# Performance work log

Measured on AMD Instinct MI355X. Metric: run time of the kernel, lower is better.

The kernel has to match this reference:

```python
import jax, jax.numpy as jnp
import numpy as np

H = 2048       # hidden_size
F = 1024       # moe_intermediate_size
E = 32         # n_routed_experts
G = 8          # n_group
TOPK_GROUP = 3
TOP_K = 6      # num_experts_per_tok
N_SHARED = 2
SCALE = 1.0    # routed_scaling_factor
B, S = 1, 2048


def setup_inputs() -> dict:
    key = jax.random.key(0)
    ks = jax.random.split(key, 8)
    std = 0.02
    return {
        "hidden_states": jax.random.normal(ks[0], (B, S, H), dtype=jnp.float32),
        "w_gate": jax.random.normal(ks[1], (E, H), dtype=jnp.float32) * std,
        "wg": jax.random.normal(ks[2], (E, H, F), dtype=jnp.float32) * std,  # stacked gate_proj
        "wu": jax.random.normal(ks[3], (E, H, F), dtype=jnp.float32) * std,  # stacked up_proj
        "wd": jax.random.normal(ks[4], (E, F, H), dtype=jnp.float32) * std,  # stacked down_proj
        "sg": jax.random.normal(ks[5], (N_SHARED * F, H), dtype=jnp.float32) * std,  # shared gate_proj
        "su": jax.random.normal(ks[6], (N_SHARED * F, H), dtype=jnp.float32) * std,  # shared up_proj
        "sd": jax.random.normal(ks[7], (H, N_SHARED * F), dtype=jnp.float32) * std,  # shared down_proj
    }


def reference(hidden_states, w_gate, wg, wu, wd, sg, su, sd):
    b, s, h = hidden_states.shape
    x = hidden_states.reshape(-1, h)                    # [T, H]
    T = x.shape[0]

    # ---- MoEGate (softmax scoring, group_limited_greedy top-k) ----
    logits = x.astype(jnp.float32) @ w_gate.T           # [T, E]
    scores = jax.nn.softmax(logits, axis=-1)
    group_scores = scores.reshape(T, G, E // G).max(axis=-1)          # [T, G]
    _, group_idx = jax.lax.top_k(group_scores, TOPK_GROUP)            # [T, topk_group]
    group_mask = jax.nn.one_hot(group_idx, G, dtype=scores.dtype).sum(axis=1)  # [T, G]
    score_mask = jnp.repeat(group_mask, E // G, axis=-1)              # [T, E]
    tmp_scores = jnp.where(score_mask > 0.5, scores, 0.0)
    topk_weight, topk_idx = jax.lax.top_k(tmp_scores, TOP_K)          # [T, K]
    # norm_topk_prob=True, top_k>1
    topk_weight = topk_weight / (topk_weight.sum(axis=-1, keepdims=True) + 1e-20) * SCALE

    # combine weights per (token, expert): scatter topk weights (indices distinct)
    combine_w = jnp.zeros((T, E), dtype=jnp.float32)
    combine_w = combine_w.at[jnp.arange(T)[:, None], topk_idx].add(topk_weight)

    # ---- routed experts: dense grouped GEMMs, weighted combine ----
    g = jnp.einsum('th,ehf->etf', x, wg)                # [E, T, F]
    u = jnp.einsum('th,ehf->etf', x, wu)                # [E, T, F]
    act = jax.nn.silu(g) * u                            # SiLU gated
    act = act * combine_w.T[:, :, None]                 # fold combine weights before down-proj
    y = jnp.einsum('etf,efh->th', act, wd)              # [T, H]

    # ---- shared experts ----
    shared = (jax.nn.silu(x @ sg.T) * (x @ su.T)) @ sd.T

    return (y + shared).reshape(b, s, h)
```

## Files before the change

kernel.cpp:

```cpp
#include <hip/hip_runtime.h>

#define HD   2048
#define FD   1024
#define NEXP 32
#define TOPK 6
#define TT   2048
#define SDIM 2048
#define NPAIR (TT*TOPK)
#define BSTR 40

typedef __bf16 bf16x8 __attribute__((ext_vector_type(8)));
typedef float  f32x4  __attribute__((ext_vector_type(4)));

#define GLOAD_LDS16(g, l) __builtin_amdgcn_global_load_lds( \
    (const __attribute__((address_space(1))) void*)(g),     \
    (__attribute__((address_space(3))) void*)(l), 16, 0, 0)

__device__ __forceinline__ ushort f2b(float f) {
  __bf16 h = (__bf16)f;
  union { __bf16 h; ushort u; } v; v.h = h;
  return v.u;
}

__device__ __forceinline__ int prow(int r) {
  return (r & ~3) | ((r + (r >> 2)) & 3);
}

__device__ __forceinline__ void argmax32(float &v, int &i) {
  #pragma unroll
  for (int m = 16; m >= 1; m >>= 1) {
    float ov = __shfl_xor(v, m, 32);
    int   oi = __shfl_xor(i, m, 32);
    if (ov > v || (ov == v && oi < i)) { v = ov; i = oi; }
  }
}

__global__ __launch_bounds__(64) void gating_kernel(
    const float* __restrict__ x, const float* __restrict__ wgate,
    int* __restrict__ topk_idx, float* __restrict__ topk_w, int* __restrict__ cnt)
{
  int t = blockIdx.x;
  int l = threadIdx.x;
  int e = l & 31;
  int half = l >> 5;
  const float* xr = x + (size_t)t * HD + half * (HD/2);
  const float* wr = wgate + (size_t)e * HD + half * (HD/2);
  float acc = 0.f;
  for (int i = 0; i < HD/2; i += 4) {
    float4 a = *(const float4*)(xr + i);
    float4 b = *(const float4*)(wr + i);
    acc += a.x*b.x + a.y*b.y + a.z*b.z + a.w*b.w;
  }
  acc += __shfl_xor(acc, 32);
  float logit = acc;
  float mx = logit;
  #pragma unroll
  for (int m = 16; m >= 1; m >>= 1) mx = fmaxf(mx, __shfl_xor(mx, m, 32));
  float p = __expf(logit - mx);
  float s = p;
  #pragma unroll
  for (int m = 16; m >= 1; m >>= 1) s += __shfl_xor(s, m, 32);
  float score = p / s;
  float gs = score;
  gs = fmaxf(gs, __shfl_xor(gs, 1, 32));
  gs = fmaxf(gs, __shfl_xor(gs, 2, 32));
  int g = e >> 2;
  float gw = gs;
  bool ingroup = false;
  for (int r = 0; r < 3; ++r) {
    float v = gw; int gi = g;
    argmax32(v, gi);
    if (g == gi) { ingroup = true; gw = -1.f; }
  }
  float ms = ingroup ? score : 0.f;
  int myrank = -1;
  float denom = 1e-20f;
  float mw = ms;
  for (int r = 0; r < 6; ++r) {
    float v = mw; int ei = e;
    argmax32(v, ei);
    denom += v;
    if (e == ei) { myrank = r; mw = -1.f; }
  }
  if (l < 32 && myrank >= 0) {
    topk_idx[t*TOPK + myrank] = e;
    topk_w  [t*TOPK + myrank] = score / denom;
    atomicAdd(&cnt[e], 1);
  }
}

__global__ void scan_kernel(const int* __restrict__ cnt, int* __restrict__ offs) {
  if (threadIdx.x == 0) {
    int o = 0;
    for (int e = 0; e < NEXP; ++e) { offs[e] = o; o += cnt[e]; }
  }
}

__global__ void fill_kernel(const int* __restrict__ topk_idx, const float* __restrict__ topk_w,
                            const int* __restrict__ offs, int* __restrict__ cur,
                            int* __restrict__ pair_tok, float* __restrict__ pair_w)
{
  int idx = blockIdx.x * blockDim.x + threadIdx.x;
  if (idx >= NPAIR) return;
  int e = topk_idx[idx];
  int p = offs[e] + atomicAdd(&cur[e], 1);
  pair_tok[p] = idx / TOPK;
  pair_w[p]   = topk_w[idx];
}

__global__ void cvt_kernel(const float* __restrict__ x, ushort* __restrict__ xb) {
  int i = blockIdx.x * blockDim.x + threadIdx.x;
  float4 v = ((const float4*)x)[i];
  ((ushort4*)xb)[i] = make_ushort4(f2b(v.x), f2b(v.y), f2b(v.z), f2b(v.w));
}

__global__ __launch_bounds__(256) void gu_routed(
    const ushort* __restrict__ xb, const float* __restrict__ wg, const float* __restrict__ wu,
    const int* __restrict__ pair_tok, const float* __restrict__ pair_w,
    const int* __restrict__ cnt, const int* __restrict__ offs,
    ushort* __restrict__ act)
{
  __shared__ ushort A[2][128*32];
  __shared__ ushort Bg[2][64*BSTR];
  __shared__ ushort Bu[2][64*BSTR];

  int bid = blockIdx.x;
  int wid = (bid & 7) * 1024 + (bid >> 3);
  int mt = wid & 15;
  int nt = (wid >> 4) & 15;
  int e  = wid >> 8;
  int ce = cnt[e];
  int m0 = mt * 128;
  if (m0 >= ce) return;
  int oe = offs[e];
  int n0 = nt * 64;
  int tid = threadIdx.x, lane = tid & 63, w = tid >> 6;

  int csrc = (lane & 3) ^ ((lane >> 3) & 3);
  const ushort* asrc[2];
  #pragma unroll
  for (int j = 0; j < 2; ++j) {
    int r = (2*w + j)*16 + (lane >> 2);
    int pi = min(m0 + r, ce - 1);
    asrc[j] = xb + (size_t)pair_tok[oe + pi] * HD + csrc * 8;
  }
  int tsel = tid >> 7;
  int ttb = tid & 127;
  int fg = ttb & 15, hg = ttb >> 4;
  const float* wsrc = (tsel ? wu : wg) + (size_t)e * HD * FD + (size_t)hg*4*FD + n0 + fg*4;

  int lm = lane & 15, lg = lane >> 4;
  int wr = w >> 1, wc = w & 1;
  int asw = (lm >> 1) & 3;

  f32x4 accg[4][2], accu[4][2];
  #pragma unroll
  for (int m = 0; m < 4; ++m)
    #pragma unroll
    for (int n = 0; n < 2; ++n) { accg[m][n] = f32x4{0,0,0,0}; accu[m][n] = f32x4{0,0,0,0}; }

  float4 rB[4];
  #define GU_ISSUE(T, BUF) do { \
    _Pragma("unroll") \
    for (int j = 0; j < 2; ++j) \
      GLOAD_LDS16(asrc[j] + (T)*32, &A[BUF][(2*w+j)*512]); \
    const float* p = wsrc + (size_t)(T)*32*FD; \
    rB[0] = *(const float4*)(p); \
    rB[1] = *(const float4*)(p + FD); \
    rB[2] = *(const float4*)(p + 2*FD); \
    rB[3] = *(const float4*)(p + 3*FD); \
  } while (0)
  #define GU_WRITE(BUF) do { \
    ushort* dst = tsel ? &Bu[BUF][0] : &Bg[BUF][0]; \
    _Pragma("unroll") \
    for (int c = 0; c < 4; ++c) { \
      int row = fg*4 + ((c + fg) & 3); \
      *(ushort4*)&dst[row*BSTR + hg*4] = \
        make_ushort4(f2b(rB[0][c]), f2b(rB[1][c]), f2b(rB[2][c]), f2b(rB[3][c])); \
    } \
  } while (0)

  GU_ISSUE(0, 0);
  asm volatile("s_waitcnt vmcnt(0)" ::: "memory");
  GU_WRITE(0);
  __syncthreads();

  int cur = 0;
  for (int t = 0; t < HD/32; ++t) {
    if (t + 1 < HD/32) GU_ISSUE(t + 1, cur ^ 1);
    bf16x8 a[4], bg[2], bu[2];
    #pragma unroll
    for (int m = 0; m < 4; ++m)
      a[m] = *(const bf16x8*)&A[cur][(wr*64 + m*16 + lm)*32 + (lg ^ asw)*8];
    #pragma unroll
    for (int n = 0; n < 2; ++n) {
      int row = prow(wc*32 + n*16 + lm);
      bg[n] = *(const bf16x8*)&Bg[cur][row*BSTR + lg*8];
      bu[n] = *(const bf16x8*)&Bu[cur][row*BSTR + lg*8];
    }
    #pragma unroll
    for (int m = 0; m < 4; ++m)
      #pragma unroll
      for (int n = 0; n < 2; ++n) {
        accg[m][n] = __builtin_amdgcn_mfma_f32_16x16x32_bf16(a[m], bg[n], accg[m][n], 0, 0, 0);
        accu[m][n] = __builtin_amdgcn_mfma_f32_16x16x32_bf16(a[m], bu[n], accu[m][n], 0, 0, 0);
      }
    if (t + 1 < HD/32) {
      asm volatile("s_waitcnt vmcnt(0)" ::: "memory");
      GU_WRITE(cur ^ 1);
    }
    __syncthreads();
    cur ^= 1;
  }
  #undef GU_ISSUE
  #undef GU_WRITE

  #pragma unroll
  for (int m = 0; m < 4; ++m) {
    #pragma unroll
    for (int j = 0; j < 4; ++j) {
      int rl = wr*64 + m*16 + lg*4 + j;
      int pi = m0 + rl;
      if (pi >= ce) continue;
      float pwv = pair_w[oe + pi];
      size_t base = (size_t)(oe + pi) * FD + n0 + wc*32;
      #pragma unroll
      for (int n = 0; n < 2; ++n) {
        float gv = accg[m][n][j];
        float uv = accu[m][n][j];
        float sv = gv / (1.f + __expf(-gv));
        act[base + n*16 + lm] = f2b(sv * uv * pwv);
      }
    }
  }
}

__global__ __launch_bounds__(256) void down_routed(
    const ushort* __restrict__ act, const float* __restrict__ wd,
    const int* __restrict__ pair_tok, const int* __restrict__ cnt, const int* __restrict__ offs,
    float* __restrict__ y)
{
  __shared__ ushort A[2][128*32];
  __shared__ ushort Bd[2][128*BSTR];

  int bid = blockIdx.x;
  int wid = (bid & 7) * 1024 + (bid >> 3);
  int mt = wid & 15;
  int nt = (wid >> 4) & 15;
  int e  = wid >> 8;
  int ce = cnt[e];
  int m0 = mt * 128;
  if (m0 >= ce) return;
  int oe = offs[e];
  int n0 = nt * 128;
  int tid = threadIdx.x, lane = tid & 63, w = tid >> 6;

  int csrc = (lane & 3) ^ ((lane >> 3) & 3);
  const ushort* asrc[2];
  #pragma unroll
  for (int j = 0; j < 2; ++j) {
    int r = (2*w + j)*16 + (lane >> 2);
    int pi = min(m0 + r, ce - 1);
    asrc[j] = act + (size_t)(oe + pi) * FD + csrc * 8;
  }
  int fg = tid & 31, hg = tid >> 5;
  const float* wsrc = wd + (size_t)e * FD * HD + (size_t)hg*4*HD + n0 + fg*4;

  int lm = lane & 15, lg = lane >> 4;
  int wr = w >> 1, wc = w & 1;
  int asw = (lm >> 1) & 3;

  f32x4 acc[4][4];
  #pragma unroll
  for (int m = 0; m < 4; ++m)
    #pragma unroll
    for (int n = 0; n < 4; ++n) acc[m][n] = f32x4{0,0,0,0};

  float4 rB[4];
  #define DN_ISSUE(T, BUF) do { \
    _Pragma("unroll") \
    for (int j = 0; j < 2; ++j) \
      GLOAD_LDS16(asrc[j] + (T)*32, &A[BUF][(2*w+j)*512]); \
    const float* p = wsrc + (size_t)(T)*32*HD; \
    rB[0] = *(const float4*)(p); \
    rB[1] = *(const float4*)(p + HD); \
    rB[2] = *(const float4*)(p + 2*HD); \
    rB[3] = *(const float4*)(p + 3*HD); \
  } while (0)
  #define DN_WRITE(BUF) do { \
    _Pragma("unroll") \
    for (int c = 0; c < 4; ++c) { \
      int row = fg*4 + ((c + fg) & 3); \
      *(ushort4*)&Bd[BUF][row*BSTR + hg*4] = \
        make_ushort4(f2b(rB[0][c]), f2b(rB[1][c]), f2b(rB[2][c]), f2b(rB[3][c])); \
    } \
  } while (0)

  DN_ISSUE(0, 0);
  asm volatile("s_waitcnt vmcnt(0)" ::: "memory");
  DN_WRITE(0);
  __syncthreads();

  int cur = 0;
  for (int t = 0; t < FD/32; ++t) {
    if (t + 1 < FD/32) DN_ISSUE(t + 1, cur ^ 1);
    bf16x8 a[4], b[4];
    #pragma unroll
    for (int m = 0; m < 4; ++m)
      a[m] = *(const bf16x8*)&A[cur][(wr*64 + m*16 + lm)*32 + (lg ^ asw)*8];
    #pragma unroll
    for (int n = 0; n < 4; ++n) {
      int row = prow(wc*64 + n*16 + lm);
      b[n] = *(const bf16x8*)&Bd[cur][row*BSTR + lg*8];
    }
    #pragma unroll
    for (int m = 0; m < 4; ++m)
      #pragma unroll
      for (int n = 0; n < 4; ++n)
        acc[m][n] = __builtin_amdgcn_mfma_f32_16x16x32_bf16(a[m], b[n], acc[m][n], 0, 0, 0);
    if (t + 1 < FD/32) {
      asm volatile("s_waitcnt vmcnt(0)" ::: "memory");
      DN_WRITE(cur ^ 1);
    }
    __syncthreads();
    cur ^= 1;
  }
  #undef DN_ISSUE
  #undef DN_WRITE

  #pragma unroll
  for (int m = 0; m < 4; ++m) {
    #pragma unroll
    for (int j = 0; j < 4; ++j) {
      int rl = wr*64 + m*16 + lg*4 + j;
      int pi = m0 + rl;
      if (pi >= ce) continue;
      int tok = pair_tok[oe + pi];
      size_t base = (size_t)tok * HD + n0 + wc*64;
      #pragma unroll
      for (int n = 0; n < 4; ++n)
        atomicAdd(&y[base + n*16 + lm], acc[m][n][j]);
    }
  }
}

__global__ __launch_bounds__(256) void shared_gu(
    const ushort* __restrict__ xb, const float* __restrict__ sg, const float* __restrict__ su,
    ushort* __restrict__ sact)
{
  __shared__ ushort A[2][128*32];
  __shared__ ushort Bg[2][64*BSTR];
  __shared__ ushort Bu[2][64*BSTR];

  int bid = blockIdx.x;
  int wid = (bid & 7) * 64 + (bid >> 3);
  int mt = wid & 15;
  int nt = wid >> 4;
  int m0 = mt * 128;
  int n0 = nt * 64;
  int tid = threadIdx.x, lane = tid & 63, w = tid >> 6;

  int csrc = (lane & 3) ^ ((lane >> 3) & 3);
  const ushort* asrc[2];
  #pragma unroll
  for (int j = 0; j < 2; ++j) {
    int r = (2*w + j)*16 + (lane >> 2);
    asrc[j] = xb + (size_t)(m0 + r) * HD + csrc * 8;
  }
  int tsel = tid >> 7;
  int ttb = tid & 127;
  int bn = ttb >> 1, bsub = ttb & 1;
  const float* bsrc = (tsel ? su : sg) + (size_t)(n0 + bn) * HD + bsub * 16;

  int lm = lane & 15, lg = lane >> 4;
  int wr = w >> 1, wc = w & 1;
  int asw = (lm >> 1) & 3;

  f32x4 accg[4][2], accu[4][2];
  #pragma unroll
  for (int m = 0; m < 4; ++m)
    #pragma unroll
    for (int n = 0; n < 2; ++n) { accg[m][n] = f32x4{0,0,0,0}; accu[m][n] = f32x4{0,0,0,0}; }

  float4 rB[4];
  #define SG_ISSUE(T, BUF) do { \
    _Pragma("unroll") \
    for (int j = 0; j < 2; ++j) \
      GLOAD_LDS16(asrc[j] + (T)*32, &A[BUF][(2*w+j)*512]); \
    const float* p = bsrc + (T)*32; \
    rB[0] = *(const float4*)(p); \
    rB[1] = *(const float4*)(p + 4); \
    rB[2] = *(const float4*)(p + 8); \
    rB[3] = *(const float4*)(p + 12); \
  } while (0)
  #define SG_WRITE(BUF) do { \
    ushort* dst = (tsel ? &Bu[BUF][0] : &Bg[BUF][0]) + bn*BSTR + bsub*16; \
    dst[0]=f2b(rB[0][0]); dst[1]=f2b(rB[0][1]); dst[2]=f2b(rB[0][2]); dst[3]=f2b(rB[0][3]); \
    dst[4]=f2b(rB[1][0]); dst[5]=f2b(rB[1][1]); dst[6]=f2b(rB[1][2]); dst[7]=f2b(rB[1][3]); \
    dst[8]=f2b(rB[2][0]); dst[9]=f2b(rB[2][1]); dst[10]=f2b(rB[2][2]); dst[11]=f2b(rB[2][3]); \
    dst[12]=f2b(rB[3][0]); dst[13]=f2b(rB[3][1]); dst[14]=f2b(rB[3][2]); dst[15]=f2b(rB[3][3]); \
  } while (0)

  SG_ISSUE(0, 0);
  asm volatile("s_waitcnt vmcnt(0)" ::: "memory");
  SG_WRITE(0);
  __syncthreads();

  int cur = 0;
  for (int t = 0; t < HD/32; ++t) {
    if (t + 1 < HD/32) SG_ISSUE(t + 1, cur ^ 1);
    bf16x8 a[4], bg[2], bu[2];
    #pragma unroll
    for (int m = 0; m < 4; ++m)
      a[m] = *(const bf16x8*)&A[cur][(wr*64 + m*16 + lm)*32 + (lg ^ asw)*8];
    #pragma unroll
    for (int n = 0; n < 2; ++n) {
      int row = wc*32 + n*16 + lm;
      bg[n] = *(const bf16x8*)&Bg[cur][row*BSTR + lg*8];
      bu[n] = *(const bf16x8*)&Bu[cur][row*BSTR + lg*8];
    }
    #pragma unroll
    for (int m = 0; m < 4; ++m)
      #pragma unroll
      for (int n = 0; n < 2; ++n) {
        accg[m][n] = __builtin_amdgcn_mfma_f32_16x16x32_bf16(a[m], bg[n], accg[m][n], 0, 0, 0);
        accu[m][n] = __builtin_amdgcn_mfma_f32_16x16x32_bf16(a[m], bu[n], accu[m][n], 0, 0, 0);
      }
    if (t + 1 < HD/32) {
      asm volatile("s_waitcnt vmcnt(0)" ::: "memory");
      SG_WRITE(cur ^ 1);
    }
    __syncthreads();
    cur ^= 1;
  }
  #undef SG_ISSUE
  #undef SG_WRITE

  #pragma unroll
  for (int m = 0; m < 4; ++m) {
    #pragma unroll
    for (int j = 0; j < 4; ++j) {
      int rl = wr*64 + m*16 + lg*4 + j;
      size_t base = (size_t)(m0 + rl) * SDIM + n0 + wc*32;
      #pragma unroll
      for (int n = 0; n < 2; ++n) {
        float gv = accg[m][n][j];
        float uv = accu[m][n][j];
        float sv = gv / (1.f + __expf(-gv));
        sact[base + n*16 + lm] = f2b(sv * uv);
      }
    }
  }
}

__global__ __launch_bounds__(256) void shared_down(
    const ushort* __restrict__ sact, const float* __restrict__ sd, float* __restrict__ y)
{
  __shared__ ushort A[2][128*32];
  __shared__ ushort Bd[2][128*BSTR];

  int bid = blockIdx.x;
  int wid = (bid & 7) * 32 + (bid >> 3);
  int mt = wid & 15;
  int nt = wid >> 4;
  int m0 = mt * 128;
  int n0 = nt * 128;
  int tid = threadIdx.x, lane = tid & 63, w = tid >> 6;

  int csrc = (lane & 3) ^ ((lane >> 3) & 3);
  const ushort* asrc[2];
  #pragma unroll
  for (int j = 0; j < 2; ++j) {
    int r = (2*w + j)*16 + (lane >> 2);
    asrc[j] = sact + (size_t)(m0 + r) * SDIM + csrc * 8;
  }
  int bn = tid >> 1, bsub = tid & 1;
  const float* bsrc = sd + (size_t)(n0 + bn) * SDIM + bsub * 16;

  int lm = lane & 15, lg = lane >> 4;
  int wr = w >> 1, wc = w & 1;
  int asw = (lm >> 1) & 3;

  f32x4 acc[4][4];
  #pragma unroll
  for (int m = 0; m < 4; ++m)
    #pragma unroll
    for (int n = 0; n < 4; ++n) acc[m][n] = f32x4{0,0,0,0};

  float4 rB[4];
  #define SD_ISSUE(T, BUF) do { \
    _Pragma("unroll") \
    for (int j = 0; j < 2; ++j) \
      GLOAD_LDS16(asrc[j] + (T)*32, &A[BUF][(2*w+j)*512]); \
    const float* p = bsrc + (T)*32; \
    rB[0] = *(const float4*)(p); \
    rB[1] = *(const float4*)(p + 4); \
    rB[2] = *(const float4*)(p + 8); \
    rB[3] = *(const float4*)(p + 12); \
  } while (0)
  #define SD_WRITE(BUF) do { \
    ushort* dst = &Bd[BUF][bn*BSTR + bsub*16]; \
    dst[0]=f2b(rB[0][0]); dst[1]=f2b(rB[0][1]); dst[2]=f2b(rB[0][2]); dst[3]=f2b(rB[0][3]); \
    dst[4]=f2b(rB[1][0]); dst[5]=f2b(rB[1][1]); dst[6]=f2b(rB[1][2]); dst[7]=f2b(rB[1][3]); \
    dst[8]=f2b(rB[2][0]); dst[9]=f2b(rB[2][1]); dst[10]=f2b(rB[2][2]); dst[11]=f2b(rB[2][3]); \
    dst[12]=f2b(rB[3][0]); dst[13]=f2b(rB[3][1]); dst[14]=f2b(rB[3][2]); dst[15]=f2b(rB[3][3]); \
  } while (0)

  SD_ISSUE(0, 0);
  asm volatile("s_waitcnt vmcnt(0)" ::: "memory");
  SD_WRITE(0);
  __syncthreads();

  int cur = 0;
  for (int t = 0; t < SDIM/32; ++t) {
    if (t + 1 < SDIM/32) SD_ISSUE(t + 1, cur ^ 1);
    bf16x8 a[4], b[4];
    #pragma unroll
    for (int m = 0; m < 4; ++m)
      a[m] = *(const bf16x8*)&A[cur][(wr*64 + m*16 + lm)*32 + (lg ^ asw)*8];
    #pragma unroll
    for (int n = 0; n < 4; ++n) {
      int row = wc*64 + n*16 + lm;
      b[n] = *(const bf16x8*)&Bd[cur][row*BSTR + lg*8];
    }
    #pragma unroll
    for (int m = 0; m < 4; ++m)
      #pragma unroll
      for (int n = 0; n < 4; ++n)
        acc[m][n] = __builtin_amdgcn_mfma_f32_16x16x32_bf16(a[m], b[n], acc[m][n], 0, 0, 0);
    if (t + 1 < SDIM/32) {
      asm volatile("s_waitcnt vmcnt(0)" ::: "memory");
      SD_WRITE(cur ^ 1);
    }
    __syncthreads();
    cur ^= 1;
  }
  #undef SD_ISSUE
  #undef SD_WRITE

  #pragma unroll
  for (int m = 0; m < 4; ++m) {
    #pragma unroll
    for (int j = 0; j < 4; ++j) {
      int rl = wr*64 + m*16 + lg*4 + j;
      size_t base = (size_t)(m0 + rl) * HD + n0 + wc*64;
      #pragma unroll
      for (int n = 0; n < 4; ++n) {
        size_t idx = base + n*16 + lm;
        y[idx] += acc[m][n][j];
      }
    }
  }
}

extern "C" void kernel_launch(void* const* d_in, const int* in_sizes, int n_in,
                              void* d_out, int out_size, void* d_ws, size_t ws_size,
                              hipStream_t stream) {
  const float* x     = (const float*)d_in[0];
  const float* wgate = (const float*)d_in[1];
  const float* wg    = (const float*)d_in[2];
  const float* wu    = (const float*)d_in[3];
  const float* wd    = (const float*)d_in[4];
  const float* sg    = (const float*)d_in[5];
  const float* su    = (const float*)d_in[6];
  const float* sd    = (const float*)d_in[7];
  float* y = (float*)d_out;
  char* ws = (char*)d_ws;

  ushort* xb   = (ushort*)(ws + 0);
  ushort* act  = (ushort*)(ws + 8388608);
  ushort* sact = (ushort*)(ws + 33554432);
  int*    tidx = (int*)  (ws + 41943040);
  float*  tw   = (float*)(ws + 41992192);
  int*    ptok = (int*)  (ws + 42041344);
  float*  pw   = (float*)(ws + 42090496);
  int*    cnt  = (int*)  (ws + 42139648);
  int*    cur  = (int*)  (ws + 42139776);
  int*    offs = (int*)  (ws + 42139904);

  hipMemsetAsync(cnt, 0, 512, stream);
  hipMemsetAsync(d_out, 0, (size_t)TT * HD * 4, stream);

  cvt_kernel<<<dim3(4096), dim3(256), 0, stream>>>(x, xb);
  gating_kernel<<<dim3(TT), dim3(64), 0, stream>>>(x, wgate, tidx, tw, cnt);
  scan_kernel<<<dim3(1), dim3(64), 0, stream>>>(cnt, offs);
  fill_kernel<<<dim3(48), dim3(256), 0, stream>>>(tidx, tw, offs, cur, ptok, pw);
  gu_routed<<<dim3(8192), dim3(256), 0, stream>>>(xb, wg, wu, ptok, pw, cnt, offs, act);
  down_routed<<<dim3(8192), dim3(256), 0, stream>>>(act, wd, ptok, cnt, offs, y);
  shared_gu<<<dim3(512), dim3(256), 0, stream>>>(xb, sg, su, sact);
  shared_down<<<dim3(256), dim3(256), 0, stream>>>(sact, sd, y);
}
```

Before: 801.5 us.

## Deepen GEMM prefetch pipeline to two stages with triple-buffered A tiles

```diff
diff --git a/kernel.cpp b/kernel.cpp
--- a/kernel.cpp
+++ b/kernel.cpp
@@ -15,6 +15,12 @@
 #define GLOAD_LDS16(g, l) __builtin_amdgcn_global_load_lds( \
     (const __attribute__((address_space(1))) void*)(g),     \
     (__attribute__((address_space(3))) void*)(l), 16, 0, 0)
+
+#define WAIT_VM6  asm volatile("s_waitcnt vmcnt(6)" ::: "memory")
+#define WAIT_VM2  asm volatile("s_waitcnt vmcnt(2)" ::: "memory")
+#define WAIT_VM0  asm volatile("s_waitcnt vmcnt(0)" ::: "memory")
+#define WAIT_LGKM asm volatile("s_waitcnt lgkmcnt(0)" ::: "memory")
+#define BAR() do { __builtin_amdgcn_s_barrier(); asm volatile("" ::: "memory"); } while (0)
 
 __device__ __forceinline__ ushort f2b(float f) {
   __bf16 h = (__bf16)f;
@@ -120,7 +126,7 @@
     const int* __restrict__ cnt, const int* __restrict__ offs,
     ushort* __restrict__ act)
 {
-  __shared__ ushort A[2][128*32];
+  __shared__ ushort A[3][128*32];
   __shared__ ushort Bg[2][64*BSTR];
   __shared__ ushort Bu[2][64*BSTR];
 
@@ -159,61 +165,72 @@
     #pragma unroll
     for (int n = 0; n < 2; ++n) { accg[m][n] = f32x4{0,0,0,0}; accu[m][n] = f32x4{0,0,0,0}; }
 
-  float4 rB[4];
-  #define GU_ISSUE(T, BUF) do { \
+  float4 rB0[4], rB1[4];
+  #define GU_ISSUE_B(T, RB) do { \
+    const float* p = wsrc + (size_t)(T)*32*FD; \
+    RB[0] = *(const float4*)(p); \
+    RB[1] = *(const float4*)(p + FD); \
+    RB[2] = *(const float4*)(p + 2*FD); \
+    RB[3] = *(const float4*)(p + 3*FD); \
+  } while (0)
+  #define GU_ISSUE_A(T, BUF) do { \
     _Pragma("unroll") \
     for (int j = 0; j < 2; ++j) \
       GLOAD_LDS16(asrc[j] + (T)*32, &A[BUF][(2*w+j)*512]); \
-    const float* p = wsrc + (size_t)(T)*32*FD; \
-    rB[0] = *(const float4*)(p); \
-    rB[1] = *(const float4*)(p + FD); \
-    rB[2] = *(const float4*)(p + 2*FD); \
-    rB[3] = *(const float4*)(p + 3*FD); \
-  } while (0)
-  #define GU_WRITE(BUF) do { \
+  } while (0)
+  #define GU_WRITE(RB, BUF) do { \
     ushort* dst = tsel ? &Bu[BUF][0] : &Bg[BUF][0]; \
     _Pragma("unroll") \
     for (int c = 0; c < 4; ++c) { \
       int row = fg*4 + ((c + fg) & 3); \
       *(ushort4*)&dst[row*BSTR + hg*4] = \
-        make_ushort4(f2b(rB[0][c]), f2b(rB[1][c]), f2b(rB[2][c]), f2b(rB[3][c])); \
+        make_ushort4(f2b(RB[0][c]), f2b(RB[1][c]), f2b(RB[2][c]), f2b(RB[3][c])); \
     } \
   } while (0)
-
-  GU_ISSUE(0, 0);
-  asm volatile("s_waitcnt vmcnt(0)" ::: "memory");
-  GU_WRITE(0);
-  __syncthreads();
-
-  int cur = 0;
-  for (int t = 0; t < HD/32; ++t) {
-    if (t + 1 < HD/32) GU_ISSUE(t + 1, cur ^ 1);
-    bf16x8 a[4], bg[2], bu[2];
-    #pragma unroll
-    for (int m = 0; m < 4; ++m)
-      a[m] = *(const bf16x8*)&A[cur][(wr*64 + m*16 + lm)*32 + (lg ^ asw)*8];
-    #pragma unroll
-    for (int n = 0; n < 2; ++n) {
-      int row = prow(wc*32 + n*16 + lm);
-      bg[n] = *(const bf16x8*)&Bg[cur][row*BSTR + lg*8];
-      bu[n] = *(const bf16x8*)&Bu[cur][row*BSTR + lg*8];
-    }
-    #pragma unroll
-    for (int m = 0; m < 4; ++m)
-      #pragma unroll
-      for (int n = 0; n < 2; ++n) {
-        accg[m][n] = __builtin_amdgcn_mfma_f32_16x16x32_bf16(a[m], bg[n], accg[m][n], 0, 0, 0);
-        accu[m][n] = __builtin_amdgcn_mfma_f32_16x16x32_bf16(a[m], bu[n], accu[m][n], 0, 0, 0);
-      }
-    if (t + 1 < HD/32) {
-      asm volatile("s_waitcnt vmcnt(0)" ::: "memory");
-      GU_WRITE(cur ^ 1);
-    }
-    __syncthreads();
-    cur ^= 1;
-  }
-  #undef GU_ISSUE
+  #define GU_COMPUTE(ABUF, BBUF) do { \
+    bf16x8 a[4], bg[2], bu[2]; \
+    _Pragma("unroll") \
+    for (int m = 0; m < 4; ++m) \
+      a[m] = *(const bf16x8*)&A[ABUF][(wr*64 + m*16 + lm)*32 + (lg ^ asw)*8]; \
+    _Pragma("unroll") \
+    for (int n = 0; n < 2; ++n) { \
+      int row = prow(wc*32 + n*16 + lm); \
+      bg[n] = *(const bf16x8*)&Bg[BBUF][row*BSTR + lg*8]; \
+      bu[n] = *(const bf16x8*)&Bu[BBUF][row*BSTR + lg*8]; \
+    } \
+    __builtin_amdgcn_s_setprio(1); \
+    _Pragma("unroll") \
+    for (int m = 0; m < 4; ++m) \
+      _Pragma("unroll") \
+      for (int n = 0; n < 2; ++n) { \
+        accg[m][n] = __builtin_amdgcn_mfma_f32_16x16x32_bf16(a[m], bg[n], accg[m][n], 0, 0, 0); \
+        accu[m][n] = __builtin_amdgcn_mfma_f32_16x16x32_bf16(a[m], bu[n], accu[m][n], 0, 0, 0); \
+      } \
+    __builtin_amdgcn_s_setprio(0); \
+  } while (0)
+
+  GU_ISSUE_B(0, rB0); GU_ISSUE_A(0, 0);
+  GU_ISSUE_B(1, rB1); GU_ISSUE_A(1, 1);
+  WAIT_VM6;
+  GU_WRITE(rB0, 0);
+  WAIT_LGKM; BAR();
+
+  for (int t = 0; t < 64; t += 2) {
+    if (t + 2 < 64) { GU_ISSUE_B(t+2, rB0); GU_ISSUE_A(t+2, (t+2)%3); }
+    GU_COMPUTE(t%3, 0);
+    if (t + 2 < 64) WAIT_VM6; else WAIT_VM2;
+    GU_WRITE(rB1, 1);
+    WAIT_LGKM; BAR();
+    if (t + 3 < 64) { GU_ISSUE_B(t+3, rB1); GU_ISSUE_A(t+3, (t+3)%3); }
+    if (t + 1 == 63) WAIT_VM0;
+    GU_COMPUTE((t+1)%3, 1);
+    if (t + 2 < 64) { WAIT_VM6; GU_WRITE(rB0, 0); WAIT_LGKM; }
+    BAR();
+  }
+  #undef GU_ISSUE_B
+  #undef GU_ISSUE_A
   #undef GU_WRITE
+  #undef GU_COMPUTE
 
   #pragma unroll
   for (int m = 0; m < 4; ++m) {
@@ -240,7 +257,7 @@
     const int* __restrict__ pair_tok, const int* __restrict__ cnt, const int* __restrict__ offs,
     float* __restrict__ y)
 {
-  __shared__ ushort A[2][128*32];
+  __shared__ ushort A[3][128*32];
   __shared__ ushort Bd[2][128*BSTR];
 
   int bid = blockIdx.x;
@@ -276,57 +293,68 @@
     #pragma unroll
     for (int n = 0; n < 4; ++n) acc[m][n] = f32x4{0,0,0,0};
 
-  float4 rB[4];
-  #define DN_ISSUE(T, BUF) do { \
+  float4 rB0[4], rB1[4];
+  #define DN_ISSUE_B(T, RB) do { \
+    const float* p = wsrc + (size_t)(T)*32*HD; \
+    RB[0] = *(const float4*)(p); \
+    RB[1] = *(const float4*)(p + HD); \
+    RB[2] = *(const float4*)(p + 2*HD); \
+    RB[3] = *(const float4*)(p + 3*HD); \
+  } while (0)
+  #define DN_ISSUE_A(T, BUF) do { \
     _Pragma("unroll") \
     for (int j = 0; j < 2; ++j) \
       GLOAD_LDS16(asrc[j] + (T)*32, &A[BUF][(2*w+j)*512]); \
-    const float* p = wsrc + (size_t)(T)*32*HD; \
-    rB[0] = *(const float4*)(p); \
-    rB[1] = *(const float4*)(p + HD); \
-    rB[2] = *(const float4*)(p + 2*HD); \
-    rB[3] = *(const float4*)(p + 3*HD); \
-  } while (0)
-  #define DN_WRITE(BUF) do { \
+  } while (0)
+  #define DN_WRITE(RB, BUF) do { \
     _Pragma("unroll") \
     for (int c = 0; c < 4; ++c) { \
       int row = fg*4 + ((c + fg) & 3); \
       *(ushort4*)&Bd[BUF][row*BSTR + hg*4] = \
-        make_ushort4(f2b(rB[0][c]), f2b(rB[1][c]), f2b(rB[2][c]), f2b(rB[3][c])); \
+        make_ushort4(f2b(RB[0][c]), f2b(RB[1][c]), f2b(RB[2][c]), f2b(RB[3][c])); \
     } \
   } while (0)
-
-  DN_ISSUE(0, 0);
-  asm volatile("s_waitcnt vmcnt(0)" ::: "memory");
-  DN_WRITE(0);
-  __syncthreads();
-
-  int cur = 0;
-  for (int t = 0; t < FD/32; ++t) {
-    if (t + 1 < FD/32) DN_ISSUE(t + 1, cur ^ 1);
-    bf16x8 a[4], b[4];
-    #pragma unroll
-    for (int m = 0; m < 4; ++m)
-      a[m] = *(const bf16x8*)&A[cur][(wr*64 + m*16 + lm)*32 + (lg ^ asw)*8];
-    #pragma unroll
-    for (int n = 0; n < 4; ++n) {
-      int row = prow(wc*64 + n*16 + lm);
-      b[n] = *(const bf16x8*)&Bd[cur][row*BSTR + lg*8];
-    }
-    #pragma unroll
-    for (int m = 0; m < 4; ++m)
-      #pragma unroll
-      for (int n = 0; n < 4; ++n)
-        acc[m][n] = __builtin_amdgcn_mfma_f32_16x16x32_bf16(a[m], b[n], acc[m][n], 0, 0, 0);
-    if (t + 1 < FD/32) {
-      asm volatile("s_waitcnt vmcnt(0)" ::: "memory");
-      DN_WRITE(cur ^ 1);
-    }
-    __syncthreads();
-    cur ^= 1;
-  }
-  #undef DN_ISSUE
+  #define DN_COMPUTE(ABUF, BBUF) do { \
+    bf16x8 a[4], b[4]; \
+    _Pragma("unroll") \
+    for (int m = 0; m < 4; ++m) \
+      a[m] = *(const bf16x8*)&A[ABUF][(wr*64 + m*16 + lm)*32 + (lg ^ asw)*8]; \
+    _Pragma("unroll") \
+    for (int n = 0; n < 4; ++n) { \
+      int row = prow(wc*64 + n*16 + lm); \
+      b[n] = *(const bf16x8*)&Bd[BBUF][row*BSTR + lg*8]; \
+    } \
+    __builtin_amdgcn_s_setprio(1); \
+    _Pragma("unroll") \
+    for (int m = 0; m < 4; ++m) \
+      _Pragma("unroll") \
+      for (int n = 0; n < 4; ++n) \
+        acc[m][n] = __builtin_amdgcn_mfma_f32_16x16x32_bf16(a[m], b[n], acc[m][n], 0, 0, 0); \
+    __builtin_amdgcn_s_setprio(0); \
+  } while (0)
+
+  DN_ISSUE_B(0, rB0); DN_ISSUE_A(0, 0);
+  DN_ISSUE_B(1, rB1); DN_ISSUE_A(1, 1);
+  WAIT_VM6;
+  DN_WRITE(rB0, 0);
+  WAIT_LGKM; BAR();
+
+  for (int t = 0; t < 32; t += 2) {
+    if (t + 2 < 32) { DN_ISSUE_B(t+2, rB0); DN_ISSUE_A(t+2, (t+2)%3); }
+    DN_COMPUTE(t%3, 0);
+    if (t + 2 < 32) WAIT_VM6; else WAIT_VM2;
+    DN_WRITE(rB1, 1);
+    WAIT_LGKM; BAR();
+    if (t + 3 < 32) { DN_ISSUE_B(t+3, rB1); DN_ISSUE_A(t+3, (t+3)%3); }
+    if (t + 1 == 31) WAIT_VM0;
+    DN_COMPUTE((t+1)%3, 1);
+    if (t + 2 < 32) { WAIT_VM6; DN_WRITE(rB0, 0); WAIT_LGKM; }
+    BAR();
+  }
+  #undef DN_ISSUE_B
+  #undef DN_ISSUE_A
   #undef DN_WRITE
+  #undef DN_COMPUTE
 
   #pragma unroll
   for (int m = 0; m < 4; ++m) {
@@ -348,7 +376,7 @@
     const ushort* __restrict__ xb, const float* __restrict__ sg, const float* __restrict__ su,
     ushort* __restrict__ sact)
 {
-  __shared__ ushort A[2][128*32];
+  __shared__ ushort A[3][128*32];
   __shared__ ushort Bg[2][64*BSTR];
   __shared__ ushort Bu[2][64*BSTR];
 
@@ -382,59 +410,70 @@
     #pragma unroll
     for (int n = 0; n < 2; ++n) { accg[m][n] = f32x4{0,0,0,0}; accu[m][n] = f32x4{0,0,0,0}; }
 
-  float4 rB[4];
-  #define SG_ISSUE(T, BUF) do { \
+  float4 rB0[4], rB1[4];
+  #define SG_ISSUE_B(T, RB) do { \
+    const float* p = bsrc + (T)*32; \
+    RB[0] = *(const float4*)(p); \
+    RB[1] = *(const float4*)(p + 4); \
+    RB[2] = *(const float4*)(p + 8); \
+    RB[3] = *(const float4*)(p + 12); \
+  } while (0)
+  #define SG_ISSUE_A(T, BUF) do { \
     _Pragma("unroll") \
     for (int j = 0; j < 2; ++j) \
       GLOAD_LDS16(asrc[j] + (T)*32, &A[BUF][(2*w+j)*512]); \
-    const float* p = bsrc + (T)*32; \
-    rB[0] = *(const float4*)(p); \
-    rB[1] = *(const float4*)(p + 4); \
-    rB[2] = *(const float4*)(p + 8); \
-    rB[3] = *(const float4*)(p + 12); \
-  } while (0)
-  #define SG_WRITE(BUF) do { \
+  } while (0)
+  #define SG_WRITE(RB, BUF) do { \
     ushort* dst = (tsel ? &Bu[BUF][0] : &Bg[BUF][0]) + bn*BSTR + bsub*16; \
-    dst[0]=f2b(rB[0][0]); dst[1]=f2b(rB[0][1]); dst[2]=f2b(rB[0][2]); dst[3]=f2b(rB[0][3]); \
-    dst[4]=f2b(rB[1][0]); dst[5]=f2b(rB[1][1]); dst[6]=f2b(rB[1][2]); dst[7]=f2b(rB[1][3]); \
-    dst[8]=f2b(rB[2][0]); dst[9]=f2b(rB[2][1]); dst[10]=f2b(rB[2][2]); dst[11]=f2b(rB[2][3]); \
-    dst[12]=f2b(rB[3][0]); dst[13]=f2b(rB[3][1]); dst[14]=f2b(rB[3][2]); dst[15]=f2b(rB[3][3]); \
-  } while (0)
-
-  SG_ISSUE(0, 0);
-  asm volatile("s_waitcnt vmcnt(0)" ::: "memory");
-  SG_WRITE(0);
-  __syncthreads();
-
-  int cur = 0;
-  for (int t = 0; t < HD/32; ++t) {
-    if (t + 1 < HD/32) SG_ISSUE(t + 1, cur ^ 1);
-    bf16x8 a[4], bg[2], bu[2];
-    #pragma unroll
-    for (int m = 0; m < 4; ++m)
-      a[m] = *(const bf16x8*)&A[cur][(wr*64 + m*16 + lm)*32 + (lg ^ asw)*8];
-    #pragma unroll
-    for (int n = 0; n < 2; ++n) {
-      int row = wc*32 + n*16 + lm;
-      bg[n] = *(const bf16x8*)&Bg[cur][row*BSTR + lg*8];
-      bu[n] = *(const bf16x8*)&Bu[cur][row*BSTR + lg*8];
-    }
-    #pragma unroll
-    for (int m = 0; m < 4; ++m)
-      #pragma unroll
-      for (int n = 0; n < 2; ++n) {
-        accg[m][n] = __builtin_amdgcn_mfma_f32_16x16x32_bf16(a[m], bg[n], accg[m][n], 0, 0, 0);
-        accu[m][n] = __builtin_amdgcn_mfma_f32_16x16x32_bf16(a[m], bu[n], accu[m][n], 0, 0, 0);
-      }
-    if (t + 1 < HD/32) {
-      asm volatile("s_waitcnt vmcnt(0)" ::: "memory");
-      SG_WRITE(cur ^ 1);
-    }
-    __syncthreads();
-    cur ^= 1;
-  }
-  #undef SG_ISSUE
+    dst[0]=f2b(RB[0][0]); dst[1]=f2b(RB[0][1]); dst[2]=f2b(RB[0][2]); dst[3]=f2b(RB[0][3]); \
+    dst[4]=f2b(RB[1][0]); dst[5]=f2b(RB[1][1]); dst[6]=f2b(RB[1][2]); dst[7]=f2b(RB[1][3]); \
+    dst[8]=f2b(RB[2][0]); dst[9]=f2b(RB[2][1]); dst[10]=f2b(RB[2][2]); dst[11]=f2b(RB[2][3]); \
+    dst[12]=f2b(RB[3][0]); dst[13]=f2b(RB[3][1]); dst[14]=f2b(RB[3][2]); dst[15]=f2b(RB[3][3]); \
+  } while (0)
+  #define SG_COMPUTE(ABUF, BBUF) do { \
+    bf16x8 a[4], bg[2], bu[2]; \
+    _Pragma("unroll") \
+    for (int m = 0; m < 4; ++m) \
+      a[m] = *(const bf16x8*)&A[ABUF][(wr*64 + m*16 + lm)*32 + (lg ^ asw)*8]; \
+    _Pragma("unroll") \
+    for (int n = 0; n < 2; ++n) { \
+      int row = wc*32 + n*16 + lm; \
+      bg[n] = *(const bf16x8*)&Bg[BBUF][row*BSTR + lg*8]; \
+      bu[n] = *(const bf16x8*)&Bu[BBUF][row*BSTR + lg*8]; \
+    } \
+    __builtin_amdgcn_s_setprio(1); \
+    _Pragma("unroll") \
+    for (int m = 0; m < 4; ++m) \
+      _Pragma("unroll") \
+      for (int n = 0; n < 2; ++n) { \
+        accg[m][n] = __builtin_amdgcn_mfma_f32_16x16x32_bf16(a[m], bg[n], accg[m][n], 0, 0, 0); \
+        accu[m][n] = __builtin_amdgcn_mfma_f32_16x16x32_bf16(a[m], bu[n], accu[m][n], 0, 0, 0); \
+      } \
+    __builtin_amdgcn_s_setprio(0); \
+  } while (0)
+
+  SG_ISSUE_B(0, rB0); SG_ISSUE_A(0, 0);
+  SG_ISSUE_B(1, rB1); SG_ISSUE_A(1, 1);
+  WAIT_VM6;
+  SG_WRITE(rB0, 0);
+  WAIT_LGKM; BAR();
+
+  for (int t = 0; t < 64; t += 2) {
+    if (t + 2 < 64) { SG_ISSUE_B(t+2, rB0); SG_ISSUE_A(t+2, (t+2)%3); }
+    SG_COMPUTE(t%3, 0);
+    if (t + 2 < 64) WAIT_VM6; else WAIT_VM2;
+    SG_WRITE(rB1, 1);
+    WAIT_LGKM; BAR();
+    if (t + 3 < 64) { SG_ISSUE_B(t+3, rB1); SG_ISSUE_A(t+3, (t+3)%3); }
+    if (t + 1 == 63) WAIT_VM0;
+    SG_COMPUTE((t+1)%3, 1);
+    if (t + 2 < 64) { WAIT_VM6; SG_WRITE(rB0, 0); WAIT_LGKM; }
+    BAR();
+  }
+  #undef SG_ISSUE_B
+  #undef SG_ISSUE_A
   #undef SG_WRITE
+  #undef SG_COMPUTE
 
   #pragma unroll
   for (int m = 0; m < 4; ++m) {
@@ -456,7 +495,7 @@
 __global__ __launch_bounds__(256) void shared_down(
     const ushort* __restrict__ sact, const float* __restrict__ sd, float* __restrict__ y)
 {
-  __shared__ ushort A[2][128*32];
+  __shared__ ushort A[3][128*32];
   __shared__ ushort Bd[2][128*BSTR];
 
   int bid = blockIdx.x;
@@ -487,56 +526,67 @@
     #pragma unroll
     for (int n = 0; n < 4; ++n) acc[m][n] = f32x4{0,0,0,0};
 
-  float4 rB[4];
-  #define SD_ISSUE(T, BUF) do { \
+  float4 rB0[4], rB1[4];
+  #define SD_ISSUE_B(T, RB) do { \
+    const float* p = bsrc + (T)*32; \
+    RB[0] = *(const float4*)(p); \
+    RB[1] = *(const float4*)(p + 4); \
+    RB[2] = *(const float4*)(p + 8); \
+    RB[3] = *(const float4*)(p + 12); \
+  } while (0)
+  #define SD_ISSUE_A(T, BUF) do { \
     _Pragma("unroll") \
     for (int j = 0; j < 2; ++j) \
       GLOAD_LDS16(asrc[j] + (T)*32, &A[BUF][(2*w+j)*512]); \
-    const float* p = bsrc + (T)*32; \
-    rB[0] = *(const float4*)(p); \
-    rB[1] = *(const float4*)(p + 4); \
-    rB[2] = *(const float4*)(p + 8); \
-    rB[3] = *(const float4*)(p + 12); \
-  } while (0)
-  #define SD_WRITE(BUF) do { \
+  } while (0)
+  #define SD_WRITE(RB, BUF) do { \
     ushort* dst = &Bd[BUF][bn*BSTR + bsub*16]; \
-    dst[0]=f2b(rB[0][0]); dst[1]=f2b(rB[0][1]); dst[2]=f2b(rB[0][2]); dst[3]=f2b(rB[0][3]); \
-    dst[4]=f2b(rB[1][0]); dst[5]=f2b(rB[1][1]); dst[6]=f2b(rB[1][2]); dst[7]=f2b(rB[1][3]); \
-    dst[8]=f2b(rB[2][0]); dst[9]=f2b(rB[2][1]); dst[10]=f2b(rB[2][2]); dst[11]=f2b(rB[2][3]); \
-    dst[12]=f2b(rB[3][0]); dst[13]=f2b(rB[3][1]); dst[14]=f2b(rB[3][2]); dst[15]=f2b(rB[3][3]); \
-  } while (0)
-
-  SD_ISSUE(0, 0);
-  asm volatile("s_waitcnt vmcnt(0)" ::: "memory");
-  SD_WRITE(0);
-  __syncthreads();
-
-  int cur = 0;
-  for (int t = 0; t < SDIM/32; ++t) {
-    if (t + 1 < SDIM/32) SD_ISSUE(t + 1, cur ^ 1);
-    bf16x8 a[4], b[4];
-    #pragma unroll
-    for (int m = 0; m < 4; ++m)
-      a[m] = *(const bf16x8*)&A[cur][(wr*64 + m*16 + lm)*32 + (lg ^ asw)*8];
-    #pragma unroll
-    for (int n = 0; n < 4; ++n) {
-      int row = wc*64 + n*16 + lm;
-      b[n] = *(const bf16x8*)&Bd[cur][row*BSTR + lg*8];
-    }
-    #pragma unroll
-    for (int m = 0; m < 4; ++m)
-      #pragma unroll
-      for (int n = 0; n < 4; ++n)
-        acc[m][n] = __builtin_amdgcn_mfma_f32_16x16x32_bf16(a[m], b[n], acc[m][n], 0, 0, 0);
-    if (t + 1 < SDIM/32) {
-      asm volatile("s_waitcnt vmcnt(0)" ::: "memory");
-      SD_WRITE(cur ^ 1);
-    }
-    __syncthreads();
-    cur ^= 1;
-  }
-  #undef SD_ISSUE
+    dst[0]=f2b(RB[0][0]); dst[1]=f2b(RB[0][1]); dst[2]=f2b(RB[0][2]); dst[3]=f2b(RB[0][3]); \
+    dst[4]=f2b(RB[1][0]); dst[5]=f2b(RB[1][1]); dst[6]=f2b(RB[1][2]); dst[7]=f2b(RB[1][3]); \
+    dst[8]=f2b(RB[2][0]); dst[9]=f2b(RB[2][1]); dst[10]=f2b(RB[2][2]); dst[11]=f2b(RB[2][3]); \
+    dst[12]=f2b(RB[3][0]); dst[13]=f2b(RB[3][1]); dst[14]=f2b(RB[3][2]); dst[15]=f2b(RB[3][3]); \
+  } while (0)
+  #define SD_COMPUTE(ABUF, BBUF) do { \
+    bf16x8 a[4], b[4]; \
+    _Pragma("unroll") \
+    for (int m = 0; m < 4; ++m) \
+      a[m] = *(const bf16x8*)&A[ABUF][(wr*64 + m*16 + lm)*32 + (lg ^ asw)*8]; \
+    _Pragma("unroll") \
+    for (int n = 0; n < 4; ++n) { \
+      int row = wc*64 + n*16 + lm; \
+      b[n] = *(const bf16x8*)&Bd[BBUF][row*BSTR + lg*8]; \
+    } \
+    __builtin_amdgcn_s_setprio(1); \
+    _Pragma("unroll") \
+    for (int m = 0; m < 4; ++m) \
+      _Pragma("unroll") \
+      for (int n = 0; n < 4; ++n) \
+        acc[m][n] = __builtin_amdgcn_mfma_f32_16x16x32_bf16(a[m], b[n], acc[m][n], 0, 0, 0); \
+    __builtin_amdgcn_s_setprio(0); \
+  } while (0)
+
+  SD_ISSUE_B(0, rB0); SD_ISSUE_A(0, 0);
+  SD_ISSUE_B(1, rB1); SD_ISSUE_A(1, 1);
+  WAIT_VM6;
+  SD_WRITE(rB0, 0);
+  WAIT_LGKM; BAR();
+
+  for (int t = 0; t < 64; t += 2) {
+    if (t + 2 < 64) { SD_ISSUE_B(t+2, rB0); SD_ISSUE_A(t+2, (t+2)%3); }
+    SD_COMPUTE(t%3, 0);
+    if (t + 2 < 64) WAIT_VM6; else WAIT_VM2;
+    SD_WRITE(rB1, 1);
+    WAIT_LGKM; BAR();
+    if (t + 3 < 64) { SD_ISSUE_B(t+3, rB1); SD_ISSUE_A(t+3, (t+3)%3); }
+    if (t + 1 == 63) WAIT_VM0;
+    SD_COMPUTE((t+1)%3, 1);
+    if (t + 2 < 64) { WAIT_VM6; SD_WRITE(rB0, 0); WAIT_LGKM; }
+    BAR();
+  }
+  #undef SD_ISSUE_B
+  #undef SD_ISSUE_A
   #undef SD_WRITE
+  #undef SD_COMPUTE
 
   #pragma unroll
   for (int m = 0; m < 4; ++m) {
```

Result: slower. 879.6 us (+9.7%).
